# Kernel tuning notes

Measured on AMD Instinct MI355X. Metric: run time of the kernel, lower is better.

Reference implementation:

```python
import jax, jax.numpy as jnp
import numpy as np

B, MAXLEN, E, H, V = 128, 20, 512, 512, 32000


def setup_inputs() -> dict:
    key = jax.random.key(0)
    ks = jax.random.split(key, 6)
    # descending-sorted lengths (pack_padded_sequence requirement), max == MAXLEN
    lengths = np.clip(MAXLEN - np.arange(B) // 8, 1, MAXLEN).astype(np.int32)
    return {
        "features": jax.random.normal(ks[0], (B, E), jnp.float32),
        "captions": jax.random.randint(ks[1], (B, MAXLEN), 0, V, jnp.int32),
        "lengths": jnp.asarray(lengths),
        "h0": jnp.zeros((B, H), jnp.float32),
        "c0": jnp.zeros((B, H), jnp.float32),
        "embed_w": jax.random.uniform(ks[2], (V, E), jnp.float32, -0.1, 0.1),
        "w_ih": jax.random.uniform(ks[3], (4 * H, E), jnp.float32, -0.05, 0.05),
        "w_hh": jax.random.uniform(ks[4], (4 * H, H), jnp.float32, -0.05, 0.05),
        "b_ih": jnp.zeros((4 * H,), jnp.float32),
        "b_hh": jnp.zeros((4 * H,), jnp.float32),
        "lin_w": jax.random.uniform(ks[5], (V, H), jnp.float32, -0.1, 0.1),
        "lin_b": jnp.zeros((V,), jnp.float32),
        "maxlen": MAXLEN,
    }


def _lstm_logits(features, captions, h0, c0, embed_w, w_ih, w_hh, b_ih, b_hh, lin_w, lin_b, maxlen):
    # teacher-forced input sequence: [features, embed(cap[:,0]), ..., embed(cap[:,maxlen-2])]
    x = jnp.concatenate(
        [features[:, None, :], jnp.take(embed_w, captions[:, : maxlen - 1], axis=0)], axis=1
    )  # [B, T, E]
    bias = b_ih + b_hh

    def cell(carry, xt):
        h, c = carry
        gates = xt @ w_ih.T + h @ w_hh.T + bias  # [B, 4H], PyTorch gate order i,f,g,o
        i, f, g, o = jnp.split(gates, 4, axis=-1)
        c = jax.nn.sigmoid(f) * c + jax.nn.sigmoid(i) * jnp.tanh(g)
        h = jax.nn.sigmoid(o) * jnp.tanh(c)
        return (h, c), h

    _, hs = jax.lax.scan(cell, (h0, c0), jnp.swapaxes(x, 0, 1))  # [T, B, H]
    return hs @ lin_w.T + lin_b  # [T, B, V] time-major logits


def _pack_indices(lengths, maxlen, batch):
    # pack_padded_sequence order: time-major, at each t keep rows with length > t
    ln = np.asarray(lengths)
    idx = np.concatenate([t * batch + np.nonzero(ln > t)[0] for t in range(maxlen)])
    return jnp.asarray(idx, jnp.int32)


def reference(features, captions, lengths, h0, c0, embed_w, w_ih, w_hh, b_ih, b_hh, lin_w, lin_b, maxlen):
    batch = captions.shape[0]
    logits = _lstm_logits(features, captions, h0, c0, embed_w, w_ih, w_hh, b_ih, b_hh, lin_w, lin_b, maxlen)
    idx = _pack_indices(lengths, maxlen, batch)
    return logits.reshape(maxlen * batch, -1)[idx]  # [sum(lengths), V]
```

## Files before the change

### kernel.cpp

```cpp
#include <hip/hip_runtime.h>
#include <math.h>

#define NB 128
#define NT 20
#define NH 512
#define NV 32000
#define NG 2048
#define NK 512

typedef __attribute__((ext_vector_type(8))) short s8v;
typedef __attribute__((ext_vector_type(4))) float f4v;
union F4 { float4 v; float f[4]; };

__device__ __forceinline__ float sigmoidf_(float x) { return 1.0f / (1.0f + expf(-x)); }

__device__ __forceinline__ ushort f2bf(float f) {
    union { float f; unsigned u; } x; x.f = f;
    unsigned r = x.u + 0x7fffu + ((x.u >> 16) & 1u);
    return (ushort)(r >> 16);
}
__device__ __forceinline__ float bf2f(ushort b) {
    union { unsigned u; float f; } x; x.u = ((unsigned)b) << 16; return x.f;
}

__device__ __forceinline__ void gload16(const void* g, void* l) {
    __builtin_amdgcn_global_load_lds((const __attribute__((address_space(1))) void*)g,
                                     (__attribute__((address_space(3))) void*)l, 16, 0, 0);
}

__device__ __forceinline__ int permrow(int r) {
    return (((r & 511) >> 5) << 7) + ((r >> 9) << 5) + (r & 31);
}

__global__ __launch_bounds__(256) void prep_kernel(
    const int* __restrict__ lengths, const float* __restrict__ b_ih,
    const float* __restrict__ b_hh, float* __restrict__ bias_r,
    int* __restrict__ idx3, int mpad3)
{
    const int tid = threadIdx.x;
    for (int j = tid; j < NG; j += 256) bias_r[permrow(j)] = b_ih[j] + b_hh[j];

    __shared__ unsigned long long s_mask[4];
    __shared__ int s_off;
    if (tid == 0) s_off = 0;
    const int len  = (tid < NB) ? lengths[tid] : 0;
    const int lane = tid & 63, wv = tid >> 6;
    __syncthreads();
    for (int t = 0; t < NT; ++t) {
        const bool flag = (len > t);
        unsigned long long bm = __ballot(flag ? 1 : 0);
        if (lane == 0) s_mask[wv] = bm;
        __syncthreads();
        int pos = s_off;
        for (int w = 0; w < wv; ++w) pos += __popcll(s_mask[w]);
        pos += __popcll(bm & ((1ull << lane) - 1ull));
        if (flag) idx3[pos] = t * NB + tid;
        __syncthreads();
        if (tid == 0) {
            int tot = 0;
            for (int w = 0; w < 4; ++w) tot += __popcll(s_mask[w]);
            s_off += tot;
        }
        __syncthreads();
    }
    for (int m = s_off + tid; m < mpad3; m += 256) idx3[m] = -1;
}

__global__ __launch_bounds__(256) void xpack_kernel(
    const float* __restrict__ features, const int* __restrict__ captions,
    const float* __restrict__ embed_w, ushort* __restrict__ Xpack)
{
    const int gid = blockIdx.x * 256 + threadIdx.x;
    const int r = gid >> 6, cc = (gid & 63) << 3;
    const int t = r >> 7, b = r & 127;
    const float* src = (t == 0) ? (features + (size_t)b * NK)
                                : (embed_w + (size_t)captions[b * NT + t - 1] * NK);
    F4 v0, v1; v0.v = *(const float4*)(src + cc); v1.v = *(const float4*)(src + cc + 4);
    s8v o;
#pragma unroll
    for (int e = 0; e < 4; ++e) { o[e] = (short)f2bf(v0.f[e]); o[e + 4] = (short)f2bf(v1.f[e]); }
    *(s8v*)(Xpack + (size_t)r * NK + cc) = o;
}

__global__ __launch_bounds__(256) void wconv_kernel(
    const float* __restrict__ in, ushort* __restrict__ outw, int n8)
{
    const int gid = blockIdx.x * 256 + threadIdx.x;
    if (gid >= n8) return;
    const int i = gid << 3;
    F4 v0, v1; v0.v = *(const float4*)(in + i); v1.v = *(const float4*)(in + i + 4);
    s8v o;
#pragma unroll
    for (int e = 0; e < 4; ++e) { o[e] = (short)f2bf(v0.f[e]); o[e + 4] = (short)f2bf(v1.f[e]); }
    *(s8v*)(outw + i) = o;
}

__global__ __launch_bounds__(256) void wconv_r_kernel(
    const float* __restrict__ in, ushort* __restrict__ outw)
{
    const int gid = blockIdx.x * 256 + threadIdx.x;
    const int row = gid >> 6, cc = (gid & 63) << 3;
    const int orow = permrow(row);
    F4 v0, v1;
    v0.v = *(const float4*)(in + (size_t)row * NK + cc);
    v1.v = *(const float4*)(in + (size_t)row * NK + cc + 4);
    s8v o;
#pragma unroll
    for (int e = 0; e < 4; ++e) { o[e] = (short)f2bf(v0.f[e]); o[e + 4] = (short)f2bf(v1.f[e]); }
    *(s8v*)(outw + (size_t)orow * NK + cc) = o;
}

__global__ __launch_bounds__(256) void split_kernel(
    const float* __restrict__ h0, const float* __restrict__ c0,
    ushort* __restrict__ Hhi, ushort* __restrict__ Hlo, float* __restrict__ cb0)
{
    const int gid = blockIdx.x * 256 + threadIdx.x;
    const int i = gid << 3;
    F4 v0, v1; v0.v = *(const float4*)(h0 + i); v1.v = *(const float4*)(h0 + i + 4);
    s8v hi, lo;
#pragma unroll
    for (int e = 0; e < 8; ++e) {
        float f = (e < 4) ? v0.f[e] : v1.f[e - 4];
        ushort h = f2bf(f);
        hi[e] = (short)h;
        lo[e] = (short)f2bf(f - bf2f(h));
    }
    *(s8v*)(Hhi + i) = hi;
    *(s8v*)(Hlo + i) = lo;
    F4 c0a, c0b; c0a.v = *(const float4*)(c0 + i); c0b.v = *(const float4*)(c0 + i + 4);
    *(float4*)(cb0 + i) = c0a.v;
    *(float4*)(cb0 + i + 4) = c0b.v;
}

__global__ __launch_bounds__(256) void gather_kernel(
    const ushort* __restrict__ Hhi, const int* __restrict__ idx3,
    ushort* __restrict__ Apack)
{
    const int gid = blockIdx.x * 256 + threadIdx.x;
    const int r = gid >> 6, cc = (gid & 63) << 3;
    const int src = idx3[r];
    s8v o;
    if (src < 0) {
#pragma unroll
        for (int e = 0; e < 8; ++e) o[e] = 0;
    } else {
        o = *(const s8v*)(Hhi + (size_t)(src + NB) * NH + cc);
    }
    *(s8v*)(Apack + (size_t)r * NK + cc) = o;
}

__global__ __launch_bounds__(256, 2) void mfma_gemm_kernel(
    const ushort* __restrict__ A, const ushort* __restrict__ B,
    const float* __restrict__ bias, float* __restrict__ C,
    int N, int Mlimit)
{
    __shared__ __align__(16) ushort lA[128 * 64];
    __shared__ __align__(16) ushort lB[128 * 64];
    const int tid = threadIdx.x;
    const int lane = tid & 63, wid = tid >> 6;
    const int m0 = blockIdx.x << 7, n0 = blockIdx.y << 7;
    const int wm = (wid & 1) << 6, wn = (wid >> 1) << 6;

    const int srow = (wid << 5) + (lane >> 3);
    const int sj   = lane & 7;

    f4v acc[4][4];
#pragma unroll
    for (int i = 0; i < 4; ++i)
#pragma unroll
        for (int j = 0; j < 4; ++j) acc[i][j] = (f4v){0.f, 0.f, 0.f, 0.f};

    const int fra = wm + (lane & 15);
    const int frb = wn + (lane & 15);
    const int kc  = lane >> 4;

    for (int k0 = 0; k0 < NK; k0 += 64) {
#pragma unroll
        for (int i = 0; i < 4; ++i) {
            const int row = srow + (i << 3);
            const int gj  = sj ^ (row & 7);
            const int lbase = (wid << 11) + (i << 9);
            gload16(A + (size_t)(m0 + row) * NK + k0 + (gj << 3), &lA[lbase]);
            gload16(B + (size_t)(n0 + row) * NK + k0 + (gj << 3), &lB[lbase]);
        }
        __syncthreads();
#pragma unroll
        for (int ks = 0; ks < 2; ++ks) {
            s8v af[4], bf[4];
            const int jc = (ks << 2) + kc;
#pragma unroll
            for (int f = 0; f < 4; ++f) {
                const int ra = fra + (f << 4);
                const int rb = frb + (f << 4);
                af[f] = *(const s8v*)&lA[ra * 64 + ((jc ^ (ra & 7)) << 3)];
                bf[f] = *(const s8v*)&lB[rb * 64 + ((jc ^ (rb & 7)) << 3)];
            }
#pragma unroll
            for (int i = 0; i < 4; ++i)
#pragma unroll
                for (int j = 0; j < 4; ++j)
                    acc[i][j] = __builtin_amdgcn_mfma_f32_16x16x32_bf16(
                        af[i], bf[j], acc[i][j], 0, 0, 0);
        }
        __syncthreads();
    }

    const int ccol = lane & 15, crow = (lane >> 4) << 2;
#pragma unroll
    for (int j = 0; j < 4; ++j) {
        const int col = n0 + wn + (j << 4) + ccol;
        const float bv = bias[col];
#pragma unroll
        for (int i = 0; i < 4; ++i) {
#pragma unroll
            for (int r = 0; r < 4; ++r) {
                const int row = m0 + wm + (i << 4) + crow + r;
                if (row < Mlimit) C[(size_t)row * N + col] = acc[i][j][r] + bv;
            }
        }
    }
}

__global__ __launch_bounds__(256, 2) void rec_step_kernel(
    const ushort* __restrict__ Ahi, const ushort* __restrict__ Alo,
    const ushort* __restrict__ Whr, const float* __restrict__ Xg,
    const float* __restrict__ cprev, float* __restrict__ cnext,
    ushort* __restrict__ Hhi_out, ushort* __restrict__ Hlo_out)
{
    __shared__ __align__(16) ushort lAh[128 * 64];
    __shared__ __align__(16) ushort lAl[128 * 64];
    __shared__ __align__(16) ushort lB[128 * 64];
    const int tid = threadIdx.x;
    const int lane = tid & 63, wid = tid >> 6;
    const int n0 = blockIdx.x << 7;
    const int wm = wid << 5;

    const int srow = (wid << 5) + (lane >> 3);
    const int sj   = lane & 7;

    f4v acc[2][8];
#pragma unroll
    for (int i = 0; i < 2; ++i)
#pragma unroll
        for (int j = 0; j < 8; ++j) acc[i][j] = (f4v){0.f, 0.f, 0.f, 0.f};

    const int fra = wm + (lane & 15);
    const int frb = lane & 15;
    const int kc  = lane >> 4;

    for (int k0 = 0; k0 < NK; k0 += 64) {
#pragma unroll
        for (int i = 0; i < 4; ++i) {
            const int row = srow + (i << 3);
            const int gj  = sj ^ (row & 7);
            const int lbase = (wid << 11) + (i << 9);
            gload16(Ahi + (size_t)row * NK + k0 + (gj << 3), &lAh[lbase]);
            gload16(Alo + (size_t)row * NK + k0 + (gj << 3), &lAl[lbase]);
            gload16(Whr + (size_t)(n0 + row) * NK + k0 + (gj << 3), &lB[lbase]);
        }
        __syncthreads();
#pragma unroll
        for (int ks = 0; ks < 2; ++ks) {
            const int jc = (ks << 2) + kc;
            s8v ah[2], al[2];
#pragma unroll
            for (int fi = 0; fi < 2; ++fi) {
                const int ra = fra + (fi << 4);
                const int off = ra * 64 + ((jc ^ (ra & 7)) << 3);
                ah[fi] = *(const s8v*)&lAh[off];
                al[fi] = *(const s8v*)&lAl[off];
            }
#pragma unroll
            for (int fj = 0; fj < 8; ++fj) {
                const int rb = frb + (fj << 4);
                s8v bf = *(const s8v*)&lB[rb * 64 + ((jc ^ (rb & 7)) << 3)];
#pragma unroll
                for (int fi = 0; fi < 2; ++fi) {
                    acc[fi][fj] = __builtin_amdgcn_mfma_f32_16x16x32_bf16(
                        ah[fi], bf, acc[fi][fj], 0, 0, 0);
                    acc[fi][fj] = __builtin_amdgcn_mfma_f32_16x16x32_bf16(
                        al[fi], bf, acc[fi][fj], 0, 0, 0);
                }
            }
        }
        __syncthreads();
    }

    const int ccol = lane & 15, crow = (lane >> 4) << 2;
#pragma unroll
    for (int fi = 0; fi < 2; ++fi) {
#pragma unroll
        for (int fj = 0; fj < 2; ++fj) {
            const int hcol = (int)(blockIdx.x << 5) + (fj << 4) + ccol;
            const int colI = n0 + (fj << 4) + ccol;
#pragma unroll
            for (int r = 0; r < 4; ++r) {
                const int b = wm + (fi << 4) + crow + r;
                const float* xg = Xg + (size_t)b * NG + colI;
                const float iv = acc[fi][fj][r]     + xg[0];
                const float fv = acc[fi][fj + 2][r] + xg[32];
                const float gv = acc[fi][fj + 4][r] + xg[64];
                const float ov = acc[fi][fj + 6][r] + xg[96];
                const float cp = cprev[(size_t)b * NH + hcol];
                const float cn = sigmoidf_(fv) * cp + sigmoidf_(iv) * tanhf(gv);
                const float hn = sigmoidf_(ov) * tanhf(cn);
                cnext[(size_t)b * NH + hcol] = cn;
                const ushort hb = f2bf(hn);
                Hhi_out[(size_t)b * NH + hcol] = hb;
                Hlo_out[(size_t)b * NH + hcol] = f2bf(hn - bf2f(hb));
            }
        }
    }
}

extern "C" void kernel_launch(void* const* d_in, const int* in_sizes, int n_in,
                              void* d_out, int out_size, void* d_ws, size_t ws_size,
                              hipStream_t stream) {
    const float* features = (const float*)d_in[0];
    const int*   captions = (const int*)d_in[1];
    const int*   lengths  = (const int*)d_in[2];
    const float* h0       = (const float*)d_in[3];
    const float* c0       = (const float*)d_in[4];
    const float* embed_w  = (const float*)d_in[5];
    const float* w_ih     = (const float*)d_in[6];
    const float* w_hh     = (const float*)d_in[7];
    const float* b_ih     = (const float*)d_in[8];
    const float* b_hh     = (const float*)d_in[9];
    const float* lin_w    = (const float*)d_in[10];
    const float* lin_b    = (const float*)d_in[11];
    float* out = (float*)d_out;

    const int M3    = out_size / NV;
    const int mt3   = (M3 + 127) >> 7;
    const int mpad3 = mt3 << 7;

    char* p = (char*)d_ws;
    auto alloc = [&](size_t bytes) { char* r = p; p += (bytes + 255) & ~(size_t)255; return r; };
    float*  Xgate = (float*)alloc(sizeof(float) * (size_t)NT * NB * NG);
    ushort* HbfA  = (ushort*)alloc(sizeof(ushort) * (size_t)(NT + 1) * NB * NH);
    ushort* HloA  = (ushort*)alloc(sizeof(ushort) * (size_t)(NT + 1) * NB * NH);
    float*  cbuf  = (float*)alloc(sizeof(float) * (size_t)2 * NB * NH);
    float*  biasr = (float*)alloc(sizeof(float) * NG);
    int*    idx3  = (int*)alloc(sizeof(int) * (size_t)NT * NB);
    ushort* Xpack = (ushort*)alloc(sizeof(ushort) * (size_t)NT * NB * NK);
    ushort* Apack = (ushort*)alloc(sizeof(ushort) * (size_t)mpad3 * NK);
    ushort* Wihr  = (ushort*)alloc(sizeof(ushort) * (size_t)NG * NK);
    ushort* Whr   = (ushort*)alloc(sizeof(ushort) * (size_t)NG * NK);
    ushort* Wlinb = (ushort*)alloc(sizeof(ushort) * (size_t)NV * NK);

    prep_kernel<<<1, 256, 0, stream>>>(lengths, b_ih, b_hh, biasr, idx3, mpad3);
    wconv_r_kernel<<<NG * 64 / 256, 256, 0, stream>>>(w_ih, Wihr);
    wconv_r_kernel<<<NG * 64 / 256, 256, 0, stream>>>(w_hh, Whr);
    wconv_kernel<<<(NV * NK / 8 + 255) / 256, 256, 0, stream>>>(lin_w, Wlinb, NV * NK / 8);
    xpack_kernel<<<NT * NB * 64 / 256, 256, 0, stream>>>(features, captions, embed_w, Xpack);
    split_kernel<<<NB * NH / 8 / 256, 256, 0, stream>>>(h0, c0, HbfA, HloA, cbuf);

    mfma_gemm_kernel<<<dim3(NT * NB / 128, NG / 128), 256, 0, stream>>>(
        Xpack, Wihr, biasr, Xgate, NG, NT * NB);

    for (int t = 0; t < NT; ++t) {
        const ushort* Ahi = HbfA + (size_t)t * NB * NH;
        const ushort* Alo = HloA + (size_t)t * NB * NH;
        const float*  cpv = cbuf + (size_t)(t & 1) * NB * NH;
        float*        cnx = cbuf + (size_t)((t + 1) & 1) * NB * NH;
        rec_step_kernel<<<16, 256, 0, stream>>>(
            Ahi, Alo, Whr, Xgate + (size_t)t * NB * NG, cpv, cnx,
            HbfA + (size_t)(t + 1) * NB * NH, HloA + (size_t)(t + 1) * NB * NH);
    }

    gather_kernel<<<mpad3 * 64 / 256, 256, 0, stream>>>(HbfA, idx3, Apack);

    mfma_gemm_kernel<<<dim3(mt3, NV / 128), 256, 0, stream>>>(
        Apack, Wlinb, lin_b, out, NV, M3);
}
```

Measured before the change: 831.6 us.

## Split recurrent step over batch halves and double-buffer LDS K-tiles

The per-timestep recurrent GEMM kernel now launches 32 blocks instead of 16, each covering 64 batch rows rather than all 128, so more CUs work on each latency-bound step. It also double-buffers the K-loop staging in shared memory, prefetching the next 64-wide K slice while MFMAs consume the current one, with explicit vmcnt waits and barriers. The cost is that each weight tile is now loaded by two blocks, and the hand-written waitcnt count must match the number of outstanding loads.

```diff
diff --git a/kernel.cpp b/kernel.cpp
--- a/kernel.cpp
+++ b/kernel.cpp
@@ -221,94 +221,95 @@
     }
 }
 
-__global__ __launch_bounds__(256, 2) void rec_step_kernel(
+__global__ __launch_bounds__(256) void rec_step2_kernel(
     const ushort* __restrict__ Ahi, const ushort* __restrict__ Alo,
     const ushort* __restrict__ Whr, const float* __restrict__ Xg,
     const float* __restrict__ cprev, float* __restrict__ cnext,
     ushort* __restrict__ Hhi_out, ushort* __restrict__ Hlo_out)
 {
-    __shared__ __align__(16) ushort lAh[128 * 64];
-    __shared__ __align__(16) ushort lAl[128 * 64];
-    __shared__ __align__(16) ushort lB[128 * 64];
+    __shared__ __align__(16) ushort lAh[2][64 * 64];
+    __shared__ __align__(16) ushort lAl[2][64 * 64];
+    __shared__ __align__(16) ushort lW [2][128 * 64];
     const int tid = threadIdx.x;
     const int lane = tid & 63, wid = tid >> 6;
-    const int n0 = blockIdx.x << 7;
-    const int wm = wid << 5;
-
-    const int srow = (wid << 5) + (lane >> 3);
-    const int sj   = lane & 7;
-
-    f4v acc[2][8];
-#pragma unroll
-    for (int i = 0; i < 2; ++i)
-#pragma unroll
-        for (int j = 0; j < 8; ++j) acc[i][j] = (f4v){0.f, 0.f, 0.f, 0.f};
-
-    const int fra = wm + (lane & 15);
-    const int frb = lane & 15;
-    const int kc  = lane >> 4;
-
-    for (int k0 = 0; k0 < NK; k0 += 64) {
-#pragma unroll
-        for (int i = 0; i < 4; ++i) {
-            const int row = srow + (i << 3);
-            const int gj  = sj ^ (row & 7);
-            const int lbase = (wid << 11) + (i << 9);
-            gload16(Ahi + (size_t)row * NK + k0 + (gj << 3), &lAh[lbase]);
-            gload16(Alo + (size_t)row * NK + k0 + (gj << 3), &lAl[lbase]);
-            gload16(Whr + (size_t)(n0 + row) * NK + k0 + (gj << 3), &lB[lbase]);
-        }
-        __syncthreads();
+    const int bh = blockIdx.x >> 4, nt = blockIdx.x & 15;
+    const int rbase = bh << 6;
+    const int n0 = nt << 7;
+
+    const int gj8 = ((lane & 7) ^ (lane >> 3)) << 3;
+    const int lrow = lane >> 3;
+
+    const int ra = (wid << 4) + (lane & 15);
+    const int rb = lane & 15;
+    const int kc = lane >> 4;
+
+    f4v acc[8];
+#pragma unroll
+    for (int j = 0; j < 8; ++j) acc[j] = (f4v){0.f, 0.f, 0.f, 0.f};
+
+    auto stage = [&](int buf, int k0) {
+#pragma unroll
+        for (int i = 0; i < 2; ++i) {
+            const int r0 = (wid << 4) + (i << 3);
+            const size_t goff = (size_t)(rbase + r0 + lrow) * NK + k0 + gj8;
+            gload16(Ahi + goff, &lAh[buf][r0 << 6]);
+            gload16(Alo + goff, &lAl[buf][r0 << 6]);
+        }
+#pragma unroll
+        for (int j = 0; j < 4; ++j) {
+            const int r0 = (wid << 5) + (j << 3);
+            gload16(Whr + (size_t)(n0 + r0 + lrow) * NK + k0 + gj8,
+                    &lW[buf][r0 << 6]);
+        }
+    };
+
+    stage(0, 0);
+    for (int it = 0; it < 8; ++it) {
+        const int cur = it & 1;
+        if (it < 7) {
+            stage(cur ^ 1, (it + 1) << 6);
+            asm volatile("s_waitcnt vmcnt(8)" ::: "memory");
+        } else {
+            asm volatile("s_waitcnt vmcnt(0)" ::: "memory");
+        }
+        asm volatile("s_barrier" ::: "memory");
 #pragma unroll
         for (int ks = 0; ks < 2; ++ks) {
             const int jc = (ks << 2) + kc;
-            s8v ah[2], al[2];
-#pragma unroll
-            for (int fi = 0; fi < 2; ++fi) {
-                const int ra = fra + (fi << 4);
-                const int off = ra * 64 + ((jc ^ (ra & 7)) << 3);
-                ah[fi] = *(const s8v*)&lAh[off];
-                al[fi] = *(const s8v*)&lAl[off];
+            const int aoff = ra * 64 + ((jc ^ (ra & 7)) << 3);
+            s8v ah = *(const s8v*)&lAh[cur][aoff];
+            s8v al = *(const s8v*)&lAl[cur][aoff];
+#pragma unroll
+            for (int fj = 0; fj < 8; ++fj) {
+                const int rw = rb + (fj << 4);
+                s8v wf = *(const s8v*)&lW[cur][rw * 64 + ((jc ^ (rw & 7)) << 3)];
+                acc[fj] = __builtin_amdgcn_mfma_f32_16x16x32_bf16(ah, wf, acc[fj], 0, 0, 0);
+                acc[fj] = __builtin_amdgcn_mfma_f32_16x16x32_bf16(al, wf, acc[fj], 0, 0, 0);
             }
-#pragma unroll
-            for (int fj = 0; fj < 8; ++fj) {
-                const int rb = frb + (fj << 4);
-                s8v bf = *(const s8v*)&lB[rb * 64 + ((jc ^ (rb & 7)) << 3)];
-#pragma unroll
-                for (int fi = 0; fi < 2; ++fi) {
-                    acc[fi][fj] = __builtin_amdgcn_mfma_f32_16x16x32_bf16(
-                        ah[fi], bf, acc[fi][fj], 0, 0, 0);
-                    acc[fi][fj] = __builtin_amdgcn_mfma_f32_16x16x32_bf16(
-                        al[fi], bf, acc[fi][fj], 0, 0, 0);
-                }
-            }
-        }
-        __syncthreads();
+        }
+        asm volatile("s_barrier" ::: "memory");
     }
 
     const int ccol = lane & 15, crow = (lane >> 4) << 2;
 #pragma unroll
-    for (int fi = 0; fi < 2; ++fi) {
-#pragma unroll
-        for (int fj = 0; fj < 2; ++fj) {
-            const int hcol = (int)(blockIdx.x << 5) + (fj << 4) + ccol;
-            const int colI = n0 + (fj << 4) + ccol;
-#pragma unroll
-            for (int r = 0; r < 4; ++r) {
-                const int b = wm + (fi << 4) + crow + r;
-                const float* xg = Xg + (size_t)b * NG + colI;
-                const float iv = acc[fi][fj][r]     + xg[0];
-                const float fv = acc[fi][fj + 2][r] + xg[32];
-                const float gv = acc[fi][fj + 4][r] + xg[64];
-                const float ov = acc[fi][fj + 6][r] + xg[96];
-                const float cp = cprev[(size_t)b * NH + hcol];
-                const float cn = sigmoidf_(fv) * cp + sigmoidf_(iv) * tanhf(gv);
-                const float hn = sigmoidf_(ov) * tanhf(cn);
-                cnext[(size_t)b * NH + hcol] = cn;
-                const ushort hb = f2bf(hn);
-                Hhi_out[(size_t)b * NH + hcol] = hb;
-                Hlo_out[(size_t)b * NH + hcol] = f2bf(hn - bf2f(hb));
-            }
+    for (int h16 = 0; h16 < 2; ++h16) {
+        const int hcol = (nt << 5) + (h16 << 4) + ccol;
+        const int xcol = n0 + (h16 << 4) + ccol;
+#pragma unroll
+        for (int r = 0; r < 4; ++r) {
+            const int b = rbase + (wid << 4) + crow + r;
+            const float* xg = Xg + (size_t)b * NG + xcol;
+            const float iv = acc[h16][r]     + xg[0];
+            const float fv = acc[h16 + 2][r] + xg[32];
+            const float gv = acc[h16 + 4][r] + xg[64];
+            const float ov = acc[h16 + 6][r] + xg[96];
+            const float cp = cprev[(size_t)b * NH + hcol];
+            const float cn = sigmoidf_(fv) * cp + sigmoidf_(iv) * tanhf(gv);
+            const float hn = sigmoidf_(ov) * tanhf(cn);
+            cnext[(size_t)b * NH + hcol] = cn;
+            const ushort hb = f2bf(hn);
+            Hhi_out[(size_t)b * NH + hcol] = hb;
+            Hlo_out[(size_t)b * NH + hcol] = f2bf(hn - bf2f(hb));
         }
     }
 }
@@ -363,7 +364,7 @@
         const ushort* Alo = HloA + (size_t)t * NB * NH;
         const float*  cpv = cbuf + (size_t)(t & 1) * NB * NH;
         float*        cnx = cbuf + (size_t)((t + 1) & 1) * NB * NH;
-        rec_step_kernel<<<16, 256, 0, stream>>>(
+        rec_step2_kernel<<<32, 256, 0, stream>>>(
             Ahi, Alo, Whr, Xgate + (size_t)t * NB * NG, cpv, cnx,
             HbfA + (size_t)(t + 1) * NB * NH, HloA + (size_t)(t + 1) * NB * NH);
     }
```

Result: faster. 691.3 us (-16.9%).
